# Kernel optimization log

Hardware: AMD Instinct MI355X
Metric: run time of the kernel (lower is better)

The kernel has to match this reference:

```python
import jax, jax.numpy as jnp
import numpy as np

KW = float(np.sqrt(3.0 * 3.0 / np.pi))  # hard-coded tube-of-response kernel width
EXT = 200.0  # half-extent of the FOV in mm (size = 400 per axis)
NLOR = 50000
NVOX = 128


def _make_lors(key, n, ext):
    # endpoints on opposite faces along the dominant (first) axis of the permuted frame
    k1, k2 = jax.random.split(key)
    yz1 = jax.random.uniform(k1, (2, n), minval=-ext, maxval=ext)
    yz2 = jax.random.uniform(k2, (2, n), minval=-ext, maxval=ext)
    x1 = jnp.full((1, n), -ext, jnp.float32)
    x2 = jnp.full((1, n), ext, jnp.float32)
    return jnp.concatenate([x1, yz1, x2, yz2], axis=0)  # [6, n]


def setup_inputs() -> dict:
    key = jax.random.key(0)
    ks = jax.random.split(key, 8)
    return {
        "image": jax.random.normal(ks[0], (NVOX, NVOX, NVOX), jnp.float32),
        "grid": jnp.array([NVOX, NVOX, NVOX], jnp.int32),
        "center": jnp.zeros((3,), jnp.float32),
        "size": jnp.full((3,), 2.0 * EXT, jnp.float32),
        "xlors": _make_lors(ks[1], NLOR, EXT),
        "ylors": _make_lors(ks[2], NLOR, EXT),
        "zlors": _make_lors(ks[3], NLOR, EXT),
        "xproj": jax.random.uniform(ks[4], (NLOR,), jnp.float32),
        "yproj": jax.random.uniform(ks[5], (NLOR,), jnp.float32),
        "zproj": jax.random.uniform(ks[6], (NLOR,), jnp.float32),
    }


def _backproject(shape, grid, center, size, lors, proj, kw):
    # Tube-of-response backprojection: march slices along axis 0, deposit a
    # Gaussian footprint (3x3 window) around the line crossing in each slice.
    N0, N1, N2 = shape
    v = size / grid.astype(jnp.float32)          # voxel size [3]
    lo = center - 0.5 * size                     # FOV lower corner [3]
    x = lo[0] + (jnp.arange(N0, dtype=jnp.float32) + 0.5) * v[0]  # slice centers [K]
    p1, p2 = lors[:, :3], lors[:, 3:6]           # [N,3]
    d = p2 - p1
    t = (x[None, :] - p1[:, :1]) / d[:, :1]      # [N,K]
    y = p1[:, 1:2] + t * d[:, 1:2]               # [N,K]
    z = p1[:, 2:3] + t * d[:, 2:3]
    fy = (y - lo[1]) / v[1] - 0.5                # fractional voxel coords
    fz = (z - lo[2]) / v[2] - 0.5
    off = jnp.arange(-1, 2)
    iy = jnp.floor(fy).astype(jnp.int32)[..., None] + off   # [N,K,3]
    iz = jnp.floor(fz).astype(jnp.int32)[..., None] + off
    cy = lo[1] + (iy.astype(jnp.float32) + 0.5) * v[1]
    cz = lo[2] + (iz.astype(jnp.float32) + 0.5) * v[2]
    dy = cy - y[..., None]
    dz = cz - z[..., None]
    d2 = dy[:, :, :, None] ** 2 + dz[:, :, None, :] ** 2    # [N,K,3,3]
    w = jnp.exp(-0.5 * d2 / (kw * kw))
    ok = ((iy >= 0) & (iy < N1))[:, :, :, None] \
       & ((iz >= 0) & (iz < N2))[:, :, None, :] \
       & ((t >= 0.0) & (t <= 1.0))[:, :, None, None]
    w = jnp.where(ok, w, 0.0) * proj[:, None, None, None]
    iyc = jnp.clip(iy, 0, N1 - 1)
    izc = jnp.clip(iz, 0, N2 - 1)
    kk = jnp.arange(N0)[None, :, None, None]
    flat = (kk * N1 + iyc[:, :, :, None]) * N2 + izc[:, :, None, :]  # [N,K,3,3]
    vol = jnp.zeros(N0 * N1 * N2, jnp.float32).at[flat.ravel()].add(w.ravel())
    return vol.reshape(N0, N1, N2)


def _perm(a, p):
    return a[jnp.array(p)]


def reference(image, grid, center, size, xlors, ylors, zlors, xproj, yproj, zproj):
    shape = image.shape
    # z-dominant LORs: base frame
    bpz = _backproject(shape, grid, center, size, zlors.T, zproj, KW)
    # x-dominant LORs: frame permuted [2,0,1], result transposed back [1,2,0]
    px = (2, 0, 1)
    shx = tuple(shape[i] for i in px)
    bpx = _backproject(shx, _perm(grid, px), _perm(center, px), _perm(size, px),
                       xlors.T, xproj, KW)
    bpxt = jnp.transpose(bpx, (1, 2, 0))
    # y-dominant LORs: frame permuted [1,0,2], result transposed back [1,0,2]
    py = (1, 0, 2)
    shy = tuple(shape[i] for i in py)
    bpy = _backproject(shy, _perm(grid, py), _perm(center, py), _perm(size, py),
                       ylors.T, yproj, KW)
    bpyt = jnp.transpose(bpy, (1, 0, 2))
    return bpxt + bpyt + bpz
```

## Files before the change

### kernel.cpp

```cpp
#include <hip/hip_runtime.h>
#include <stdint.h>

#define NVOX 128
#define VOL  (NVOX * NVOX * NVOX)
#define SLICE (NVOX * NVOX)
#define WPS  (SLICE / 2)
#define PVOL (VOL / 2)
#define NTHREADS 512
#define NS 2
#define LO   (-200.0f)
#define VPIX 3.125f
#define INV_V 0.32f

#define NEGL   (-0.25179782f)
#define NEG2VL (-1.5737362f)
#define NEGV2L (-2.4589628f)
#define C2     (0.0330793f)
#define FSCALE 1024.0f
#define INV_FSCALE (1.0f / 1024.0f)
#define MAGIC  12582912.0f

#define TROWS 132
#define TWORDS 66
#define TSZ (TROWS * TWORDS)

__global__ __launch_bounds__(NTHREADS) void bp_fused(
    const float4* __restrict__ pk,
    const float*  __restrict__ pz,
    const float*  __restrict__ py,
    const float*  __restrict__ px,
    unsigned* __restrict__ vols,
    int nlor)
{
    __shared__ unsigned tile[TSZ];
    const int k     = blockIdx.x;
    const int chunk = blockIdx.y;
    const int dir   = blockIdx.z;

    const float* proj = (dir == 0) ? pz : (dir == 1) ? py : px;
    const float4* p   = pk + (size_t)dir * nlor;
    unsigned* vol = vols + ((size_t)dir * NS + chunk) * PVOL;
    const int n0 = (int)(((long long)chunk * nlor) / NS);
    const int n1 = (int)(((long long)(chunk + 1) * nlor) / NS);

    for (int i = threadIdx.x; i < TSZ; i += NTHREADS) tile[i] = 0u;
    __syncthreads();

    const float t = (k + 0.5f) * 0.0078125f;

    auto deposit = [&](int n) {
        float4 v  = p[n];
        float prF = proj[n] * FSCALE;
        float y = fmaf(t, v.z, v.x);
        float z = fmaf(t, v.w, v.y);
        float fy = fmaf(y, INV_V, 63.5f);
        float fz = fmaf(z, INV_V, 63.5f);
        float ffy = floorf(fy), ffz = floorf(fz);
        float dy0 = fmaf(ffy, VPIX, -201.5625f - y);
        float dz0 = fmaf(ffz, VPIX, -201.5625f - z);

        float wy0 = exp2f(NEGL * dy0 * dy0) * prF;
        float uy  = exp2f(fmaf(NEG2VL, dy0, NEGV2L));
        float wy1 = wy0 * uy;
        float wy2 = wy1 * (uy * C2);
        float wz0 = exp2f(NEGL * dz0 * dz0);
        float uz  = exp2f(fmaf(NEG2VL, dz0, NEGV2L));
        float wz1 = wz0 * uz;
        float wz2 = wz1 * (uz * C2);
        float wyv[3] = { wy0, wy1, wy2 };

        int row = (int)ffy + 1;
        int col = (int)ffz + 1;
        int sh  = (col & 1) << 4;
        int w0  = row * TWORDS + (col >> 1);

        #pragma unroll
        for (int oy = 0; oy < 3; ++oy) {
            float w = wyv[oy];
            unsigned f0 = __float_as_uint(fmaf(w, wz0, MAGIC));
            unsigned f1 = __float_as_uint(fmaf(w, wz1, MAGIC));
            unsigned f2 = __float_as_uint(fmaf(w, wz2, MAGIC));
            unsigned long long V =
                (unsigned long long)((f0 & 0xFFFFu) | (f1 << 16)) |
                ((unsigned long long)(f2 & 0xFFFFu) << 32);
            V <<= sh;
            int b = w0 + oy * TWORDS;
            atomicAdd(&tile[b],     (unsigned)V);
            atomicAdd(&tile[b + 1], (unsigned)(V >> 32));
        }
    };

    int n = n0 + (int)threadIdx.x;
    for (; n + NTHREADS < n1; n += 2 * NTHREADS) {
        deposit(n);
        deposit(n + NTHREADS);
    }
    if (n < n1) deposit(n);
    __syncthreads();

    unsigned* dst = vol + (size_t)k * WPS;
    for (int i = threadIdx.x; i < WPS; i += NTHREADS) {
        int iy = i >> 6, w = i & 63;
        dst[i] = tile[(iy + 2) * TWORDS + w + 1];
    }
}

__global__ __launch_bounds__(256) void prep(
    const float* __restrict__ lz, const float* __restrict__ ly,
    const float* __restrict__ lx, float4* __restrict__ pk, int nlor)
{
    int n = blockIdx.x * 256 + threadIdx.x;
    if (n >= nlor) return;
    const float* l = (blockIdx.y == 0) ? lz : (blockIdx.y == 1) ? ly : lx;
    float y1 = l[1 * nlor + n], z1 = l[2 * nlor + n];
    float y2 = l[4 * nlor + n], z2 = l[5 * nlor + n];
    pk[(size_t)blockIdx.y * nlor + n] = make_float4(y1, z1, y2 - y1, z2 - z1);
}

__global__ __launch_bounds__(256) void merge_all(
    float2* __restrict__ out,
    const unsigned* __restrict__ vz,
    const unsigned* __restrict__ vy,
    const unsigned* __restrict__ vx)
{
    __shared__ float T[64][65];
    int a  = blockIdx.x;
    int tb = (blockIdx.y & 1) * 64;
    int tc = (blockIdx.y >> 1) * 64;
    int wb = threadIdx.x & 31;
    int r0 = threadIdx.x >> 5;

    for (int cc = r0; cc < 64; cc += 8) {
        size_t wi = ((size_t)(tc + cc) * NVOX + a) * 64 + (tb >> 1) + wb;
        unsigned wA = vx[wi], wB = vx[PVOL + wi];
        T[cc][2 * wb]     = (float)((wA & 0xFFFFu) + (wB & 0xFFFFu)) * INV_FSCALE;
        T[cc][2 * wb + 1] = (float)((wA >> 16) + (wB >> 16)) * INV_FSCALE;
    }
    __syncthreads();
    for (int bb = r0; bb < 64; bb += 8) {
        int b = tb + bb;
        size_t zi = ((size_t)a * NVOX + b) * 64 + (tc >> 1) + wb;
        size_t yi = ((size_t)b * NVOX + a) * 64 + (tc >> 1) + wb;
        unsigned zA = vz[zi], zB = vz[PVOL + zi];
        unsigned yA = vy[yi], yB = vy[PVOL + yi];
        float s0 = (float)((zA & 0xFFFFu) + (zB & 0xFFFFu) +
                           (yA & 0xFFFFu) + (yB & 0xFFFFu)) * INV_FSCALE
                 + T[2 * wb][bb];
        float s1 = (float)((zA >> 16) + (zB >> 16) +
                           (yA >> 16) + (yB >> 16)) * INV_FSCALE
                 + T[2 * wb + 1][bb];
        out[zi] = make_float2(s0, s1);
    }
}

template<int DIR>
__global__ __launch_bounds__(256) void bp_direct(
    const float* __restrict__ lors, const float* __restrict__ proj,
    float* __restrict__ out, int nlor)
{
    int tid = blockIdx.x * 256 + threadIdx.x;
    int k = tid & (NVOX - 1);
    int n = tid >> 7;
    if (n >= nlor) return;

    float p1x = lors[0 * nlor + n];
    float p1y = lors[1 * nlor + n];
    float p1z = lors[2 * nlor + n];
    float p2x = lors[3 * nlor + n];
    float p2y = lors[4 * nlor + n];
    float p2z = lors[5 * nlor + n];
    float pr  = proj[n];

    float xk = LO + (k + 0.5f) * VPIX;
    float t  = (xk - p1x) / (p2x - p1x);
    if (t < 0.0f || t > 1.0f) return;

    float y = p1y + t * (p2y - p1y);
    float z = p1z + t * (p2z - p1z);
    float fy = (y - LO) * INV_V - 0.5f;
    float fz = (z - LO) * INV_V - 0.5f;
    int iy0 = (int)floorf(fy) - 1;
    int iz0 = (int)floorf(fz) - 1;

    const float NEG = -0.17453292519943295f;
    float wy[3], wz[3];
    #pragma unroll
    for (int o = 0; o < 3; ++o) {
        int iy = iy0 + o;
        float dy = (iy + 0.5f) * VPIX + LO - y;
        wy[o] = (iy >= 0 && iy < NVOX) ? __expf(NEG * dy * dy) * pr : 0.0f;
        int iz = iz0 + o;
        float dz = (iz + 0.5f) * VPIX + LO - z;
        wz[o] = (iz >= 0 && iz < NVOX) ? __expf(NEG * dz * dz) : 0.0f;
    }
    #pragma unroll
    for (int oy = 0; oy < 3; ++oy) {
        if (wy[oy] == 0.0f) continue;
        int iy = iy0 + oy;
        #pragma unroll
        for (int oz = 0; oz < 3; ++oz) {
            if (wz[oz] == 0.0f) continue;
            int iz = iz0 + oz;
            int idx = (DIR == 0) ? (iy * NVOX + iz) * NVOX + k
                    : (DIR == 1) ? (iy * NVOX + k) * NVOX + iz
                                 : (k * NVOX + iy) * NVOX + iz;
            atomicAdd(&out[idx], wy[oy] * wz[oz]);
        }
    }
}

extern "C" void kernel_launch(void* const* d_in, const int* in_sizes, int n_in,
                              void* d_out, int out_size, void* d_ws, size_t ws_size,
                              hipStream_t stream) {
    const float* xlors = (const float*)d_in[4];
    const float* ylors = (const float*)d_in[5];
    const float* zlors = (const float*)d_in[6];
    const float* xproj = (const float*)d_in[7];
    const float* yproj = (const float*)d_in[8];
    const float* zproj = (const float*)d_in[9];
    float* out = (float*)d_out;
    const int nlor = in_sizes[7];
    const size_t volsB = 6 * (size_t)PVOL * sizeof(unsigned);
    const size_t pkB   = 3 * (size_t)nlor * sizeof(float4);

    if (ws_size >= volsB + pkB && (nlor & 1) == 0) {
        unsigned* vols = (unsigned*)d_ws;
        float4* pk = (float4*)((char*)d_ws + volsB);

        dim3 pgrid((nlor + 255) / 256, 3);
        prep<<<pgrid, 256, 0, stream>>>(zlors, ylors, xlors, pk, nlor);

        dim3 bgrid(NVOX, NS, 3);
        bp_fused<<<bgrid, NTHREADS, 0, stream>>>(pk, zproj, yproj, xproj,
                                                 vols, nlor);

        dim3 mgrid(NVOX, 4);
        merge_all<<<mgrid, 256, 0, stream>>>(
            (float2*)out, vols, vols + 2 * (size_t)PVOL, vols + 4 * (size_t)PVOL);
    } else {
        hipMemsetAsync(d_out, 0, (size_t)VOL * sizeof(float), stream);
        const int blocks = (nlor * NVOX + 255) / 256;
        bp_direct<0><<<blocks, 256, 0, stream>>>(xlors, xproj, out, nlor);
        bp_direct<1><<<blocks, 256, 0, stream>>>(ylors, yproj, out, nlor);
        bp_direct<2><<<blocks, 256, 0, stream>>>(zlors, zproj, out, nlor);
    }
}
```

Baseline: 64.18 us.

## Split z/y LORs into three chunks and x into two, prescale projections in prep

The backprojection grid goes from 128x2x3 blocks to 128x8: z- and y-dominant LORs get three partial volumes each, x-dominant LORs keep two. The aim is more blocks in flight and fewer LORs per block, set by an occupancy hint of 8 blocks per CU, since each block processes one slice. Projections are multiplied by the fixed-point scale once in prep rather than in every slice block, and the deposit loop is unrolled by four. The cost is two more partial volumes to write and then read back in merge, and each 16-bit packed field now sums fewer LORs per partial volume.

```diff
diff --git a/kernel.cpp b/kernel.cpp
--- a/kernel.cpp
+++ b/kernel.cpp
@@ -7,7 +7,7 @@
 #define WPS  (SLICE / 2)
 #define PVOL (VOL / 2)
 #define NTHREADS 512
-#define NS 2
+#define NREP 8
 #define LO   (-200.0f)
 #define VPIX 3.125f
 #define INV_V 0.32f
@@ -24,24 +24,24 @@
 #define TWORDS 66
 #define TSZ (TROWS * TWORDS)
 
-__global__ __launch_bounds__(NTHREADS) void bp_fused(
+__global__ __launch_bounds__(NTHREADS, 8) void bp_fused(
     const float4* __restrict__ pk,
-    const float*  __restrict__ pz,
-    const float*  __restrict__ py,
-    const float*  __restrict__ px,
+    const float*  __restrict__ projF,
     unsigned* __restrict__ vols,
     int nlor)
 {
     __shared__ unsigned tile[TSZ];
-    const int k     = blockIdx.x;
-    const int chunk = blockIdx.y;
-    const int dir   = blockIdx.z;
-
-    const float* proj = (dir == 0) ? pz : (dir == 1) ? py : px;
+    const int k  = blockIdx.x;
+    const int gy = blockIdx.y;
+    const int dir   = (gy < 3) ? 0 : (gy < 6) ? 1 : 2;
+    const int chunk = gy - dir * 3;
+    const int nsd   = (dir == 2) ? 2 : 3;
+
     const float4* p   = pk + (size_t)dir * nlor;
-    unsigned* vol = vols + ((size_t)dir * NS + chunk) * PVOL;
-    const int n0 = (int)(((long long)chunk * nlor) / NS);
-    const int n1 = (int)(((long long)(chunk + 1) * nlor) / NS);
+    const float*  prf = projF + (size_t)dir * nlor;
+    unsigned* vol = vols + (size_t)gy * PVOL;
+    const int n0 = (int)(((long long)chunk * nlor) / nsd);
+    const int n1 = (int)(((long long)(chunk + 1) * nlor) / nsd);
 
     for (int i = threadIdx.x; i < TSZ; i += NTHREADS) tile[i] = 0u;
     __syncthreads();
@@ -50,7 +50,7 @@
 
     auto deposit = [&](int n) {
         float4 v  = p[n];
-        float prF = proj[n] * FSCALE;
+        float prF = prf[n];
         float y = fmaf(t, v.z, v.x);
         float z = fmaf(t, v.w, v.y);
         float fy = fmaf(y, INV_V, 63.5f);
@@ -91,11 +91,13 @@
     };
 
     int n = n0 + (int)threadIdx.x;
-    for (; n + NTHREADS < n1; n += 2 * NTHREADS) {
+    for (; n + 3 * NTHREADS < n1; n += 4 * NTHREADS) {
         deposit(n);
         deposit(n + NTHREADS);
-    }
-    if (n < n1) deposit(n);
+        deposit(n + 2 * NTHREADS);
+        deposit(n + 3 * NTHREADS);
+    }
+    for (; n < n1; n += NTHREADS) deposit(n);
     __syncthreads();
 
     unsigned* dst = vol + (size_t)k * WPS;
@@ -107,23 +109,28 @@
 
 __global__ __launch_bounds__(256) void prep(
     const float* __restrict__ lz, const float* __restrict__ ly,
-    const float* __restrict__ lx, float4* __restrict__ pk, int nlor)
+    const float* __restrict__ lx,
+    const float* __restrict__ pz, const float* __restrict__ py,
+    const float* __restrict__ px,
+    float4* __restrict__ pk, float* __restrict__ projF, int nlor)
 {
     int n = blockIdx.x * 256 + threadIdx.x;
     if (n >= nlor) return;
-    const float* l = (blockIdx.y == 0) ? lz : (blockIdx.y == 1) ? ly : lx;
+    const float* l  = (blockIdx.y == 0) ? lz : (blockIdx.y == 1) ? ly : lx;
+    const float* pr = (blockIdx.y == 0) ? pz : (blockIdx.y == 1) ? py : px;
     float y1 = l[1 * nlor + n], z1 = l[2 * nlor + n];
     float y2 = l[4 * nlor + n], z2 = l[5 * nlor + n];
     pk[(size_t)blockIdx.y * nlor + n] = make_float4(y1, z1, y2 - y1, z2 - z1);
+    projF[(size_t)blockIdx.y * nlor + n] = pr[n] * FSCALE;
 }
 
 __global__ __launch_bounds__(256) void merge_all(
-    float2* __restrict__ out,
-    const unsigned* __restrict__ vz,
-    const unsigned* __restrict__ vy,
-    const unsigned* __restrict__ vx)
+    float2* __restrict__ out, const unsigned* __restrict__ vols)
 {
     __shared__ float T[64][65];
+    const unsigned* vz = vols;
+    const unsigned* vy = vols + 3 * (size_t)PVOL;
+    const unsigned* vx = vols + 6 * (size_t)PVOL;
     int a  = blockIdx.x;
     int tb = (blockIdx.y & 1) * 64;
     int tc = (blockIdx.y >> 1) * 64;
@@ -132,24 +139,30 @@
 
     for (int cc = r0; cc < 64; cc += 8) {
         size_t wi = ((size_t)(tc + cc) * NVOX + a) * 64 + (tb >> 1) + wb;
-        unsigned wA = vx[wi], wB = vx[PVOL + wi];
-        T[cc][2 * wb]     = (float)((wA & 0xFFFFu) + (wB & 0xFFFFu)) * INV_FSCALE;
-        T[cc][2 * wb + 1] = (float)((wA >> 16) + (wB >> 16)) * INV_FSCALE;
+        unsigned lo = 0, hi = 0;
+        #pragma unroll
+        for (int r = 0; r < 2; ++r) {
+            unsigned w = vx[(size_t)r * PVOL + wi];
+            lo += w & 0xFFFFu; hi += w >> 16;
+        }
+        T[cc][2 * wb]     = (float)lo * INV_FSCALE;
+        T[cc][2 * wb + 1] = (float)hi * INV_FSCALE;
     }
     __syncthreads();
     for (int bb = r0; bb < 64; bb += 8) {
         int b = tb + bb;
         size_t zi = ((size_t)a * NVOX + b) * 64 + (tc >> 1) + wb;
         size_t yi = ((size_t)b * NVOX + a) * 64 + (tc >> 1) + wb;
-        unsigned zA = vz[zi], zB = vz[PVOL + zi];
-        unsigned yA = vy[yi], yB = vy[PVOL + yi];
-        float s0 = (float)((zA & 0xFFFFu) + (zB & 0xFFFFu) +
-                           (yA & 0xFFFFu) + (yB & 0xFFFFu)) * INV_FSCALE
-                 + T[2 * wb][bb];
-        float s1 = (float)((zA >> 16) + (zB >> 16) +
-                           (yA >> 16) + (yB >> 16)) * INV_FSCALE
-                 + T[2 * wb + 1][bb];
-        out[zi] = make_float2(s0, s1);
+        unsigned lo = 0, hi = 0;
+        #pragma unroll
+        for (int r = 0; r < 3; ++r) {
+            unsigned wz = vz[(size_t)r * PVOL + zi];
+            unsigned wy = vy[(size_t)r * PVOL + yi];
+            lo += (wz & 0xFFFFu) + (wy & 0xFFFFu);
+            hi += (wz >> 16) + (wy >> 16);
+        }
+        out[zi] = make_float2((float)lo * INV_FSCALE + T[2 * wb][bb],
+                              (float)hi * INV_FSCALE + T[2 * wb + 1][bb]);
     }
 }
 
@@ -220,23 +233,24 @@
     const float* zproj = (const float*)d_in[9];
     float* out = (float*)d_out;
     const int nlor = in_sizes[7];
-    const size_t volsB = 6 * (size_t)PVOL * sizeof(unsigned);
+    const size_t volsB = (size_t)NREP * PVOL * sizeof(unsigned);
     const size_t pkB   = 3 * (size_t)nlor * sizeof(float4);
-
-    if (ws_size >= volsB + pkB && (nlor & 1) == 0) {
+    const size_t pfB   = 3 * (size_t)nlor * sizeof(float);
+
+    if (ws_size >= volsB + pkB + pfB && (nlor & 1) == 0) {
         unsigned* vols = (unsigned*)d_ws;
-        float4* pk = (float4*)((char*)d_ws + volsB);
+        float4* pk    = (float4*)((char*)d_ws + volsB);
+        float*  projF = (float*)((char*)d_ws + volsB + pkB);
 
         dim3 pgrid((nlor + 255) / 256, 3);
-        prep<<<pgrid, 256, 0, stream>>>(zlors, ylors, xlors, pk, nlor);
-
-        dim3 bgrid(NVOX, NS, 3);
-        bp_fused<<<bgrid, NTHREADS, 0, stream>>>(pk, zproj, yproj, xproj,
-                                                 vols, nlor);
+        prep<<<pgrid, 256, 0, stream>>>(zlors, ylors, xlors,
+                                        zproj, yproj, xproj, pk, projF, nlor);
+
+        dim3 bgrid(NVOX, NREP);
+        bp_fused<<<bgrid, NTHREADS, 0, stream>>>(pk, projF, vols, nlor);
 
         dim3 mgrid(NVOX, 4);
-        merge_all<<<mgrid, 256, 0, stream>>>(
-            (float2*)out, vols, vols + 2 * (size_t)PVOL, vols + 4 * (size_t)PVOL);
+        merge_all<<<mgrid, 256, 0, stream>>>((float2*)out, vols);
     } else {
         hipMemsetAsync(d_out, 0, (size_t)VOL * sizeof(float), stream);
         const int blocks = (nlor * NVOX + 255) / 256;
```

Result: no change. 64.77 us (+0.9%).
